# Kernel tuning notes

Hardware: AMD Instinct MI355X
Metric: run time of the kernel (lower is better)

Reference implementation:

```python
import jax, jax.numpy as jnp
import numpy as np

FEAT_STRIDE = 16
PRE_NMS = 6000
POST_NMS = 300
NMS_THRESH = 0.7


def _whctrs(a):
    w = a[2] - a[0] + 1.0
    h = a[3] - a[1] + 1.0
    return w, h, a[0] + 0.5 * (w - 1), a[1] + 0.5 * (h - 1)

def _mkanchors(ws, hs, xc, yc):
    return np.stack([xc - 0.5 * (ws - 1), yc - 0.5 * (hs - 1),
                     xc + 0.5 * (ws - 1), yc + 0.5 * (hs - 1)], axis=1)

def _ratio_enum(anchor, ratios):
    w, h, xc, yc = _whctrs(anchor)
    size = w * h
    ws = np.round(np.sqrt(size / ratios))
    hs = np.round(ws * ratios)
    return _mkanchors(ws, hs, xc, yc)

def _scale_enum(anchor, scales):
    w, h, xc, yc = _whctrs(anchor)
    return _mkanchors(w * scales, h * scales, xc, yc)

def generate_anchors(base_size=16, ratios=np.array([0.5, 1.0, 2.0]), scales=np.array([8, 16, 32])):
    base = np.array([1, 1, base_size, base_size], dtype=np.float64) - 1
    ra = _ratio_enum(base, np.asarray(ratios, np.float64))
    return np.vstack([_scale_enum(ra[i], np.asarray(scales, np.float64)) for i in range(ra.shape[0])])


def setup_inputs() -> dict:
    key = jax.random.key(0)
    k1, k2 = jax.random.split(key)
    B, A, H, W = 8, 9, 64, 64
    scores = jax.random.normal(k1, (B, 2 * A, H, W), jnp.float32)
    bbox_deltas = jax.random.normal(k2, (B, 4 * A, H, W), jnp.float32)
    anchors = jnp.asarray(generate_anchors(16), jnp.float32)  # [9, 4]
    return {"scores": scores, "bbox_deltas": bbox_deltas, "anchors": anchors,
            "image_width": 1024, "image_height": 1024}


def _nms_keep(iou, thresh):
    # greedy NMS on score-sorted boxes given a full IoU matrix
    n = iou.shape[0]
    idx = jnp.arange(n)
    def body(i, keep):
        sup = keep[i] & (iou[i] > thresh) & (idx > i)
        return keep & ~sup
    return jax.lax.fori_loop(0, n, body, jnp.ones((n,), bool))


def _nms_one(boxes):  # boxes [PRE_NMS, 4], sorted by score desc
    b = jax.lax.stop_gradient(boxes)
    area = (b[:, 2] - b[:, 0] + 1.0) * (b[:, 3] - b[:, 1] + 1.0)
    iw = jnp.clip(jnp.minimum(b[:, None, 2], b[None, :, 2]) -
                  jnp.maximum(b[:, None, 0], b[None, :, 0]) + 1.0, 0.0)
    ih = jnp.clip(jnp.minimum(b[:, None, 3], b[None, :, 3]) -
                  jnp.maximum(b[:, None, 1], b[None, :, 1]) + 1.0, 0.0)
    inter = iw * ih
    iou = inter / (area[:, None] + area[None, :] - inter)
    keep = _nms_keep(iou, NMS_THRESH)
    # compact kept boxes to the front, pad with zeros (fixed shape)
    rank = jnp.cumsum(keep) - 1
    dest = jnp.where(keep, rank, PRE_NMS)  # suppressed -> dump row
    out = jnp.zeros((PRE_NMS + 1, 4), boxes.dtype).at[dest].set(boxes)
    return out[:POST_NMS]


def _forward(scores, bbox_deltas, anchors, image_width, image_height):
    B = scores.shape[0]
    A = anchors.shape[0]
    H, W = scores.shape[2], scores.shape[3]
    fg = scores[:, A:, :, :]                                   # [B, A, H, W]
    # shifted anchor grid
    mx, my = jnp.meshgrid(jnp.arange(W) * FEAT_STRIDE, jnp.arange(H) * FEAT_STRIDE)
    shifts = jnp.stack([mx.ravel(), my.ravel(), mx.ravel(), my.ravel()], 1).astype(scores.dtype)
    all_anchors = (shifts[:, None, :] + anchors[None, :, :]).reshape(-1, 4)  # [K*A, 4]
    deltas = bbox_deltas.transpose(0, 2, 3, 1).reshape(B, -1, 4)             # [B, K*A, 4]
    sc = fg.transpose(0, 2, 3, 1).reshape(B, -1)                             # [B, K*A]
    # bbox_transform_inv
    aw = all_anchors[:, 2] - all_anchors[:, 0] + 1.0
    ah = all_anchors[:, 3] - all_anchors[:, 1] + 1.0
    acx = all_anchors[:, 0] + 0.5 * aw
    acy = all_anchors[:, 1] + 0.5 * ah
    pcx = deltas[..., 0] * aw + acx
    pcy = deltas[..., 1] * ah + acy
    pw = jnp.exp(deltas[..., 2]) * aw
    ph = jnp.exp(deltas[..., 3]) * ah
    # clip to image
    x1 = jnp.clip(pcx - 0.5 * pw, 0.0, image_width - 1)
    y1 = jnp.clip(pcy - 0.5 * ph, 0.0, image_height - 1)
    x2 = jnp.clip(pcx + 0.5 * pw, 0.0, image_width - 1)
    y2 = jnp.clip(pcy + 0.5 * ph, 0.0, image_height - 1)
    proposals = jnp.stack([x1, y1, x2, y2], -1)                 # [B, K*A, 4]
    # per-image pre-NMS top-k by score
    _, order = jax.lax.top_k(sc, PRE_NMS)
    boxes = jnp.take_along_axis(proposals, order[..., None], axis=1)  # [B, PRE, 4]
    props = jax.lax.map(_nms_one, boxes)                        # [B, POST, 4]
    bidx = jnp.broadcast_to(jnp.arange(B, dtype=props.dtype)[:, None, None], (B, POST_NMS, 1))
    return jnp.concatenate([bidx, props], axis=-1)              # [B, POST, 5]


def reference(scores, bbox_deltas, anchors, image_width, image_height):
    return _forward(scores, bbox_deltas, anchors, image_width, image_height)
```

## Files before the change

kernel.cpp:

```cpp
#include <hip/hip_runtime.h>
#include <math.h>

#pragma clang fp contract(off)

#define BB 8
#define AA 9
#define NPIX 4096
#define NN (NPIX*AA)
#define PRE 6000
#define POST 300
#define SELCAP 7000
#define TMAX 10111
#define HZW 5120

#define RA 0x3F000000u
#define RB 0x41000000u
__device__ __forceinline__ unsigned key_bin2(unsigned k) {
    return (k < RA) ? (k >> 17) : (8064u + ((k - RA) >> 14));
}

#define SMEM_BYTES 65536

__device__ __forceinline__ unsigned score_key(float s) {
    unsigned fb = __float_as_uint(s);
    unsigned u = (fb & 0x80000000u) ? ~fb : (fb | 0x80000000u);
    return ~u;
}

__device__ __forceinline__ unsigned phalf(unsigned v, unsigned bin) {
    return (v >> ((bin & 1) << 4)) & 0xFFFFu;
}

__device__ __forceinline__ bool iou_gt(float ax1, float ay1, float ax2, float ay2, float aa,
                                       float bx1_, float by1_, float bx2_, float by2_, float ab) {
    float xx1 = fmaxf(ax1, bx1_);
    float yy1 = fmaxf(ay1, by1_);
    float xx2 = fminf(ax2, bx2_);
    float yy2 = fminf(ay2, by2_);
    float iw = fmaxf(xx2 - xx1 + 1.0f, 0.0f);
    float ih = fmaxf(yy2 - yy1 + 1.0f, 0.0f);
    float inter = iw * ih;
    float uni = (aa + ab) - inter;
    return (double)inter >= 0x1.666667p-1 * (double)uni;
}

__device__ __forceinline__ void decode_box(int g, const unsigned short* sorted16,
                                           const float* anch, const float* deltas_b,
                                           float fw, float fh, float4* bx, float* ar) {
    unsigned idx = sorted16[(g < PRE) ? g : (PRE - 1)];
    int a = (int)(idx % AA);
    int pix = (int)(idx / AA);
    int wq = pix & 63, hq = pix >> 6;
    float sx = (float)(wq * 16), sy = (float)(hq * 16);
    float ax1 = anch[a * 4 + 0] + sx, ay1 = anch[a * 4 + 1] + sy;
    float ax2 = anch[a * 4 + 2] + sx, ay2 = anch[a * 4 + 3] + sy;
    float aw = ax2 - ax1 + 1.0f, ah = ay2 - ay1 + 1.0f;
    float acx = ax1 + 0.5f * aw, acy = ay1 + 0.5f * ah;
    const float* dp = deltas_b + (size_t)(a * 4) * NPIX + pix;
    float d0 = dp[0], d1 = dp[NPIX], d2 = dp[2 * NPIX], d3 = dp[3 * NPIX];
    float pcx = d0 * aw + acx, pcy = d1 * ah + acy;
    float pw = expf(d2) * aw, ph = expf(d3) * ah;
    float x1 = fminf(fmaxf(pcx - 0.5f * pw, 0.0f), fw);
    float y1 = fminf(fmaxf(pcy - 0.5f * ph, 0.0f), fh);
    float x2 = fminf(fmaxf(pcx + 0.5f * pw, 0.0f), fw);
    float y2 = fminf(fmaxf(pcy + 0.5f * ph, 0.0f), fh);
    *bx = make_float4(x1, y1, x2, y2);
    *ar = (x2 - x1 + 1.0f) * (y2 - y1 + 1.0f);
}

__global__ __launch_bounds__(1024) void proposal_kernel(const float* __restrict__ scores,
                                                        const float* __restrict__ deltas,
                                                        const float* __restrict__ anchors,
                                                        const int* __restrict__ imw,
                                                        const int* __restrict__ imh,
                                                        float* __restrict__ out) {
    __shared__ __align__(16) unsigned char smem[SMEM_BYTES];
    unsigned*       hist32 = (unsigned*)smem;
    unsigned*       keyh   = (unsigned*)(smem + 20480);
    unsigned short* idxl   = (unsigned short*)(smem + 48512);
    unsigned*       scal   = (unsigned*)(smem + 65344);
    unsigned short* sorted16 = (unsigned short*)(smem + 20480);
    float4*         kb4  = (float4*)smem;
    float*          kba  = (float*)(smem + 4800);
    float4*         cnd4 = (float4*)(smem + 6016);
    float*          cnda = (float*)(smem + 8064);
    unsigned long long* srow  = (unsigned long long*)(smem + 8576);
    unsigned long long* deadw = (unsigned long long*)(smem + 9088);
    float*          anch = (float*)(smem + 9216);

    int b = blockIdx.x;
    int tid = threadIdx.x;
    int wave = tid >> 6, lane = tid & 63;
    const float* sc = scores + (size_t)(b * (2 * AA) + AA) * NPIX;
    const float4* sc4 = (const float4*)sc;
    const float* deltas_b = deltas + (size_t)b * (4 * AA) * NPIX;
    float fw = (float)(imw[0] - 1);
    float fh = (float)(imh[0] - 1);

    for (int j = tid; j < HZW; j += 1024) hist32[j] = 0;
    __syncthreads();
    #pragma unroll
    for (int q = 0; q < 9; ++q) {
        float4 v = sc4[(q << 10) + tid];
        unsigned k0 = score_key(v.x), k1 = score_key(v.y);
        unsigned k2 = score_key(v.z), k3 = score_key(v.w);
        if (k0 < RB) { unsigned b0 = key_bin2(k0); atomicAdd(&hist32[b0 >> 1], 1u << ((b0 & 1) << 4)); }
        if (k1 < RB) { unsigned b1 = key_bin2(k1); atomicAdd(&hist32[b1 >> 1], 1u << ((b1 & 1) << 4)); }
        if (k2 < RB) { unsigned b2 = key_bin2(k2); atomicAdd(&hist32[b2 >> 1], 1u << ((b2 & 1) << 4)); }
        if (k3 < RB) { unsigned b3 = key_bin2(k3); atomicAdd(&hist32[b3 >> 1], 1u << ((b3 & 1) << 4)); }
    }
    __syncthreads();

    unsigned ssum = 0;
    const unsigned* hw = hist32 + tid * 16;
    if (tid < 320) {
        #pragma unroll
        for (int j = 0; j < 16; ++j) { unsigned w = hw[j]; ssum += (w & 0xFFFFu) + (w >> 16); }
    }
    unsigned x = ssum;
    #pragma unroll
    for (int d = 1; d < 64; d <<= 1) {
        unsigned y = __shfl_up(x, (unsigned)d, 64);
        if (lane >= d) x += y;
    }
    if (lane == 63 && wave < 5) scal[wave] = x;
    __syncthreads();
    unsigned wexcl = 0;
    #pragma unroll
    for (int w = 0; w < 5; ++w) if (w < wave) wexcl += scal[w];
    unsigned gexcl = wexcl + (x - ssum);
    unsigned gincl = gexcl + ssum;
    if (tid == 319) { scal[16] = TMAX; scal[17] = gincl; }
    __syncthreads();
    if (tid < 320 && gexcl <= (PRE - 1) && (PRE - 1) < gincl) {
        unsigned c = gexcl, T = tid * 32, tot = gincl;
        bool f = false;
        for (int j = 0; j < 32 && !f; ++j) {
            unsigned d = phalf(hw[j >> 1], (unsigned)j);
            if ((PRE - 1) < c + d) { T = tid * 32 + j; tot = c + d; f = true; }
            c += d;
        }
        scal[16] = T;
        scal[17] = tot;
    }
    __syncthreads();
    unsigned T = scal[16];
    if (T > TMAX) T = TMAX;
    unsigned cnt = scal[17];
    if (cnt > SELCAP) cnt = SELCAP;

    if ((unsigned)(tid * 32) <= T) {
        unsigned run = gexcl;
        unsigned* wv = hist32 + tid * 16;
        #pragma unroll
        for (int j = 0; j < 16; ++j) {
            unsigned v = wv[j];
            unsigned c0 = v & 0xFFFFu, c1 = v >> 16;
            wv[j] = run | ((run + c0) << 16);
            run += c0 + c1;
        }
    }
    __syncthreads();

    #pragma unroll
    for (int q = 0; q < 9; ++q) {
        float4 v = sc4[(q << 10) + tid];
        #pragma unroll
        for (int c = 0; c < 4; ++c) {
            float s = (c == 0) ? v.x : (c == 1) ? v.y : (c == 2) ? v.z : v.w;
            unsigned k = score_key(s);
            if (k < RB) {
                unsigned bin = key_bin2(k);
                if (bin <= T) {
                    unsigned old = atomicAdd(&hist32[bin >> 1], 1u << ((bin & 1) << 4));
                    unsigned pos = phalf(old, bin);
                    if (pos < SELCAP) {
                        keyh[pos] = k;
                        int pix = (tid << 2) + c;
                        idxl[pos] = (unsigned short)(pix * AA + q);
                    }
                }
            }
        }
    }
    __syncthreads();

    unsigned rnk8[8], id8[8];
    #pragma unroll
    for (int m = 0; m < 8; ++m) {
        int s = (m << 10) + tid;
        rnk8[m] = 0xFFFFFFFFu;
        if (s < (int)cnt) {
            unsigned k = keyh[s];
            unsigned id = idxl[s];
            unsigned bin = key_bin2(k);
            unsigned start = bin ? phalf(hist32[(bin - 1) >> 1], bin - 1) : 0u;
            unsigned end = phalf(hist32[bin >> 1], bin);
            if (end > cnt) end = cnt;
            if (start > end) start = end;
            unsigned rank = start;
            for (unsigned j = start; j < end; ++j) {
                unsigned kj = keyh[j];
                rank += (kj < k) ? 1u : 0u;
                if (kj == k) rank += ((unsigned)idxl[j] < id) ? 1u : 0u;
            }
            rnk8[m] = rank;
            id8[m] = id;
        }
    }
    __syncthreads();
    #pragma unroll
    for (int m = 0; m < 8; ++m)
        if (rnk8[m] < PRE) sorted16[rnk8[m]] = (unsigned short)id8[m];
    if (tid < 36) anch[tid] = anchors[tid];
    __syncthreads();

    if (tid < 64) {
        float4 bx; float ar;
        decode_box(tid, sorted16, anch, deltas_b, fw, fh, &bx, &ar);
        cnd4[tid] = bx; cnda[tid] = ar;
    }
    __syncthreads();

    int cur = 0, K = 0, p = 0;
    for (;;) {
        float4 mc = cnd4[p * 64 + lane];
        float ma = cnda[p * 64 + lane];

        float4 nb; float na;
        if (wave == 8)
            decode_box(cur + 64 + lane, sorted16, anch, deltas_b, fw, fh, &nb, &na);

        bool dead = (cur + lane >= PRE);
        for (int k = wave; k < K; k += 16) {
            float4 kv = kb4[k];
            float ka = kba[k];
            dead = dead || iou_gt(kv.x, kv.y, kv.z, kv.w, ka, mc.x, mc.y, mc.z, mc.w, ma);
        }
        unsigned long long db = __ballot(dead);
        if (lane == 0) deadw[wave] = db;

        #pragma unroll
        for (int q2 = 0; q2 < 4; ++q2) {
            int j = (q2 << 4) + wave;
            float4 cj = cnd4[p * 64 + j];
            float aj = cnda[p * 64 + j];
            bool g = (lane < j) && iou_gt(mc.x, mc.y, mc.z, mc.w, ma,
                                          cj.x, cj.y, cj.z, cj.w, aj);
            unsigned long long bl = __ballot(g);
            if (lane == 0) srow[j] = bl;
        }
        if (wave == 8) {
            cnd4[(p ^ 1) * 64 + lane] = nb;
            cnda[(p ^ 1) * 64 + lane] = na;
        }
        __syncthreads();

        unsigned long long dk = deadw[0];
        #pragma unroll
        for (int w = 1; w < 16; ++w) dk |= deadw[w];
        unsigned long long row = srow[lane];
        unsigned long long live = ~dk;
        unsigned long long keptb = 0ULL;
        int allowed = POST - K;
        while (live) {
            int f = __ffsll((long long)live) - 1;
            keptb |= (1ULL << f);
            if (__popcll(keptb) >= allowed) break;
            bool die = (row >> f) & 1ULL;
            unsigned long long dbl = __ballot(die);
            live &= ~(dbl | (1ULL << f));
        }
        int nkeep = __popcll(keptb);
        int take = (nkeep < allowed) ? nkeep : allowed;

        if (wave == 0 && ((keptb >> lane) & 1ULL)) {
            int rnk = __popcll(keptb & ((1ULL << lane) - 1ULL));
            if (rnk < take) { kb4[K + rnk] = mc; kba[K + rnk] = ma; }
        }
        K += take;
        cur += 64;
        if (K >= POST || cur >= PRE) break;
        p ^= 1;
        __syncthreads();
    }

    __syncthreads();
    for (int idx = tid; idx < POST * 5; idx += 1024) {
        int row_ = idx / 5;
        int col = idx - row_ * 5;
        float val = 0.0f;
        if (row_ < K) {
            float4 v = kb4[row_];
            val = (col == 0) ? (float)b : (col == 1) ? v.x : (col == 2) ? v.y
                : (col == 3) ? v.z : v.w;
        }
        out[(size_t)b * POST * 5 + idx] = val;
    }
}

extern "C" void kernel_launch(void* const* d_in, const int* in_sizes, int n_in,
                              void* d_out, int out_size, void* d_ws, size_t ws_size,
                              hipStream_t stream) {
    const float* scores  = (const float*)d_in[0];
    const float* deltas  = (const float*)d_in[1];
    const float* anchors = (const float*)d_in[2];
    const int*   imw     = (const int*)d_in[3];
    const int*   imh     = (const int*)d_in[4];
    float* out = (float*)d_out;

    proposal_kernel<<<BB, 1024, 0, stream>>>(scores, deltas, anchors, imw, imh, out);
}
```

Baseline: 146.7 us.

## Software-pipeline box decode and remove second barrier in NMS loop

Splits box decoding into a global-load issue phase and a compute phase, so wave 8 prefetches the deltas for the chunk after next while finishing the decode for the next chunk. The aim is to hide global memory latency inside the serial NMS loop. Wave 8 now does no kept-box IoU checks, so those are spread across the other 15 waves. deadw and srow are double-buffered so the trailing __syncthreads per iteration can go, leaving one lightweight LDS-wait barrier. All waves now write kept boxes redundantly, and correctness depends on the double-buffered LDS regions not overlapping other data.

```diff
diff --git a/kernel.cpp b/kernel.cpp
--- a/kernel.cpp
+++ b/kernel.cpp
@@ -44,9 +44,10 @@
     return (double)inter >= 0x1.666667p-1 * (double)uni;
 }
 
-__device__ __forceinline__ void decode_box(int g, const unsigned short* sorted16,
-                                           const float* anch, const float* deltas_b,
-                                           float fw, float fh, float4* bx, float* ar) {
+__device__ __forceinline__ void dec_issue(int g, const unsigned short* sorted16,
+                                          const float* anch, const float* deltas_b,
+                                          float* aw, float* ah, float* acx, float* acy,
+                                          float* d0, float* d1, float* d2, float* d3) {
     unsigned idx = sorted16[(g < PRE) ? g : (PRE - 1)];
     int a = (int)(idx % AA);
     int pix = (int)(idx / AA);
@@ -54,10 +55,16 @@
     float sx = (float)(wq * 16), sy = (float)(hq * 16);
     float ax1 = anch[a * 4 + 0] + sx, ay1 = anch[a * 4 + 1] + sy;
     float ax2 = anch[a * 4 + 2] + sx, ay2 = anch[a * 4 + 3] + sy;
-    float aw = ax2 - ax1 + 1.0f, ah = ay2 - ay1 + 1.0f;
-    float acx = ax1 + 0.5f * aw, acy = ay1 + 0.5f * ah;
+    float w_ = ax2 - ax1 + 1.0f, h_ = ay2 - ay1 + 1.0f;
+    *aw = w_; *ah = h_;
+    *acx = ax1 + 0.5f * w_; *acy = ay1 + 0.5f * h_;
     const float* dp = deltas_b + (size_t)(a * 4) * NPIX + pix;
-    float d0 = dp[0], d1 = dp[NPIX], d2 = dp[2 * NPIX], d3 = dp[3 * NPIX];
+    *d0 = dp[0]; *d1 = dp[NPIX]; *d2 = dp[2 * NPIX]; *d3 = dp[3 * NPIX];
+}
+
+__device__ __forceinline__ void dec_finish(float aw, float ah, float acx, float acy,
+                                           float d0, float d1, float d2, float d3,
+                                           float fw, float fh, float4* bx, float* ar) {
     float pcx = d0 * aw + acx, pcy = d1 * ah + acy;
     float pw = expf(d2) * aw, ph = expf(d3) * ah;
     float x1 = fminf(fmaxf(pcx - 0.5f * pw, 0.0f), fw);
@@ -66,6 +73,20 @@
     float y2 = fminf(fmaxf(pcy + 0.5f * ph, 0.0f), fh);
     *bx = make_float4(x1, y1, x2, y2);
     *ar = (x2 - x1 + 1.0f) * (y2 - y1 + 1.0f);
+}
+
+__device__ __forceinline__ void decode_box(int g, const unsigned short* sorted16,
+                                           const float* anch, const float* deltas_b,
+                                           float fw, float fh, float4* bx, float* ar) {
+    float aw, ah, acx, acy, d0, d1, d2, d3;
+    dec_issue(g, sorted16, anch, deltas_b, &aw, &ah, &acx, &acy, &d0, &d1, &d2, &d3);
+    dec_finish(aw, ah, acx, acy, d0, d1, d2, d3, fw, fh, bx, ar);
+}
+
+__device__ __forceinline__ void bar_lds() {
+    asm volatile("s_waitcnt lgkmcnt(0)" ::: "memory");
+    __builtin_amdgcn_s_barrier();
+    asm volatile("" ::: "memory");
 }
 
 __global__ __launch_bounds__(1024) void proposal_kernel(const float* __restrict__ scores,
@@ -85,8 +106,8 @@
     float4*         cnd4 = (float4*)(smem + 6016);
     float*          cnda = (float*)(smem + 8064);
     unsigned long long* srow  = (unsigned long long*)(smem + 8576);
-    unsigned long long* deadw = (unsigned long long*)(smem + 9088);
-    float*          anch = (float*)(smem + 9216);
+    unsigned long long* deadw = (unsigned long long*)(smem + 9600);
+    float*          anch = (float*)(smem + 9856);
 
     int b = blockIdx.x;
     int tid = threadIdx.x;
@@ -215,30 +236,45 @@
     if (tid < 36) anch[tid] = anchors[tid];
     __syncthreads();
 
+    float s_aw = 0.f, s_ah = 0.f, s_acx = 0.f, s_acy = 0.f;
+    float s_d0 = 0.f, s_d1 = 0.f, s_d2 = 0.f, s_d3 = 0.f;
+
     if (tid < 64) {
         float4 bx; float ar;
         decode_box(tid, sorted16, anch, deltas_b, fw, fh, &bx, &ar);
         cnd4[tid] = bx; cnda[tid] = ar;
     }
-    __syncthreads();
-
-    int cur = 0, K = 0, p = 0;
+    if (wave == 8)
+        dec_issue(64 + lane, sorted16, anch, deltas_b,
+                  &s_aw, &s_ah, &s_acx, &s_acy, &s_d0, &s_d1, &s_d2, &s_d3);
+    __syncthreads();
+
+    int cur = 0, K = 0, p = 0, pb = 0;
     for (;;) {
         float4 mc = cnd4[p * 64 + lane];
         float ma = cnda[p * 64 + lane];
 
-        float4 nb; float na;
-        if (wave == 8)
-            decode_box(cur + 64 + lane, sorted16, anch, deltas_b, fw, fh, &nb, &na);
+        if (wave == 8) {
+            float4 nb; float na;
+            dec_finish(s_aw, s_ah, s_acx, s_acy, s_d0, s_d1, s_d2, s_d3,
+                       fw, fh, &nb, &na);
+            cnd4[(p ^ 1) * 64 + lane] = nb;
+            cnda[(p ^ 1) * 64 + lane] = na;
+            dec_issue(cur + 128 + lane, sorted16, anch, deltas_b,
+                      &s_aw, &s_ah, &s_acx, &s_acy, &s_d0, &s_d1, &s_d2, &s_d3);
+        }
 
         bool dead = (cur + lane >= PRE);
-        for (int k = wave; k < K; k += 16) {
-            float4 kv = kb4[k];
-            float ka = kba[k];
-            dead = dead || iou_gt(kv.x, kv.y, kv.z, kv.w, ka, mc.x, mc.y, mc.z, mc.w, ma);
+        if (wave != 8) {
+            int w15 = (wave < 8) ? wave : (wave - 1);
+            for (int k = w15; k < K; k += 15) {
+                float4 kv = kb4[k];
+                float ka = kba[k];
+                dead = dead || iou_gt(kv.x, kv.y, kv.z, kv.w, ka, mc.x, mc.y, mc.z, mc.w, ma);
+            }
         }
         unsigned long long db = __ballot(dead);
-        if (lane == 0) deadw[wave] = db;
+        if (lane == 0) deadw[pb * 16 + wave] = db;
 
         #pragma unroll
         for (int q2 = 0; q2 < 4; ++q2) {
@@ -248,18 +284,15 @@
             bool g = (lane < j) && iou_gt(mc.x, mc.y, mc.z, mc.w, ma,
                                           cj.x, cj.y, cj.z, cj.w, aj);
             unsigned long long bl = __ballot(g);
-            if (lane == 0) srow[j] = bl;
-        }
-        if (wave == 8) {
-            cnd4[(p ^ 1) * 64 + lane] = nb;
-            cnda[(p ^ 1) * 64 + lane] = na;
-        }
-        __syncthreads();
-
-        unsigned long long dk = deadw[0];
-        #pragma unroll
-        for (int w = 1; w < 16; ++w) dk |= deadw[w];
-        unsigned long long row = srow[lane];
+            if (lane == 0) srow[pb * 64 + j] = bl;
+        }
+
+        bar_lds();
+
+        unsigned long long dk = deadw[pb * 16 + 0];
+        #pragma unroll
+        for (int w = 1; w < 16; ++w) dk |= deadw[pb * 16 + w];
+        unsigned long long row = srow[pb * 64 + lane];
         unsigned long long live = ~dk;
         unsigned long long keptb = 0ULL;
         int allowed = POST - K;
@@ -274,15 +307,14 @@
         int nkeep = __popcll(keptb);
         int take = (nkeep < allowed) ? nkeep : allowed;
 
-        if (wave == 0 && ((keptb >> lane) & 1ULL)) {
+        if ((keptb >> lane) & 1ULL) {
             int rnk = __popcll(keptb & ((1ULL << lane) - 1ULL));
             if (rnk < take) { kb4[K + rnk] = mc; kba[K + rnk] = ma; }
         }
         K += take;
         cur += 64;
         if (K >= POST || cur >= PRE) break;
-        p ^= 1;
-        __syncthreads();
+        p ^= 1; pb ^= 1;
     }
 
     __syncthreads();
```

Result: no change. 145.7 us (-0.7%).
